# Kernel optimization log

Measured on AMD Instinct MI355X. Metric: run time of the kernel, lower is better.

The kernel has to match this reference:

```python
import jax, jax.numpy as jnp
import numpy as np

N_NODES = 100000
N_EDGES = 1600000
IN_CH = 128
OUT_CH = 128
EDGE_DIM = 6
STATE_DIM = 5


def setup_inputs() -> dict:
    key = jax.random.key(0)
    k = jax.random.split(key, 8)
    x = jax.random.normal(k[0], (N_NODES, IN_CH), dtype=jnp.float32)
    edge_index = jax.random.randint(k[1], (2, N_EDGES), 0, N_NODES, dtype=jnp.int64)
    edge_attr = jax.random.normal(k[2], (N_EDGES, EDGE_DIM), dtype=jnp.float32)
    global_state = jax.random.normal(k[3], (N_NODES, STATE_DIM), dtype=jnp.float32)
    # learned params (glorot init for weights, zero bias like torch default-ish)
    d_neg_in = IN_CH + EDGE_DIM + STATE_DIM
    d_root_in = IN_CH + STATE_DIM
    s_neg = jnp.sqrt(6.0 / (d_neg_in + OUT_CH))
    s_root = jnp.sqrt(6.0 / (d_root_in + OUT_CH))
    W_neg = jax.random.uniform(k[4], (d_neg_in, OUT_CH), jnp.float32, -s_neg, s_neg)
    b_neg = jax.random.uniform(k[5], (OUT_CH,), jnp.float32, -0.05, 0.05)
    W_root = jax.random.uniform(k[6], (d_root_in, OUT_CH), jnp.float32, -s_root, s_root)
    b_root = jax.random.uniform(k[7], (OUT_CH,), jnp.float32, -0.05, 0.05)
    return {"x": x, "edge_index": edge_index, "edge_attr": edge_attr,
            "global_state": global_state, "W_neg": W_neg, "b_neg": b_neg,
            "W_root": W_root, "b_root": b_root}


def reference(x, edge_index, edge_attr, global_state, W_neg, b_neg, W_root, b_root):
    # x: [N, C], global_state: [N, S]
    xs = jnp.concatenate([x, global_state], axis=1)            # [N, C+S]
    src = xs[edge_index[1]]                                    # gather: [E, C+S]
    x_adj = jnp.concatenate([src, edge_attr], axis=1)          # [E, C+S+Ed]
    x_adj = jax.nn.elu(x_adj @ W_neg + b_neg)                  # [E, O]
    neg_sum = jax.ops.segment_sum(x_adj, edge_index[0], num_segments=xs.shape[0])  # [N, O]
    x_out = jax.nn.elu(xs @ W_root + b_root) + neg_sum         # [N, O]
    return x_out
```

## Files before the change

kernel.cpp:

```cpp
#include <hip/hip_runtime.h>
#include <hip/hip_bf16.h>
#include <math.h>

#define N_NODES 100000
#define N_EDGES 1600000
#define IN_CH 128
#define OUT_CH 128
#define EDGE_DIM 6
#define STATE_DIM 5
#define XS_DIM 133
#define KPAD 160
#define NKSTEP 5
#define ASTRIDE 168
#define NBLK 391
#define N_CHUNKS 25000

typedef short s16x8 __attribute__((ext_vector_type(8)));
typedef float f32x4 __attribute__((ext_vector_type(4)));

static __device__ __forceinline__ unsigned short f2bf(float f) {
    __hip_bfloat16 h = __float2bfloat16(f);
    return *reinterpret_cast<unsigned short*>(&h);
}
static __device__ __forceinline__ float bflo(unsigned u) {
    return __uint_as_float(u << 16);
}
static __device__ __forceinline__ float bfhi(unsigned u) {
    return __uint_as_float(u & 0xffff0000u);
}

__global__ __launch_bounds__(64) void repack_w(
    const float* __restrict__ Wneg, const float* __restrict__ Wroot,
    unsigned short* __restrict__ Pneg, unsigned short* __restrict__ Proot)
{
    int b = blockIdx.x;
    int mat = b / 40, r = b % 40;
    int kk = r / 8, nt = r % 8;
    int lane = threadIdx.x;
    const float* W = mat ? Wroot : Wneg;
    unsigned short* P = mat ? Proot : Pneg;
    int n = nt * 16 + (lane & 15);
    int kb = kk * 32 + (lane >> 4) * 8;
    unsigned short v[8];
#pragma unroll
    for (int j = 0; j < 8; ++j) {
        int k = kb + j;
        v[j] = (k < XS_DIM) ? f2bf(W[k * 128 + n]) : (unsigned short)0;
    }
    *(s16x8*)(P + ((size_t)(kk * 8 + nt) * 64 + lane) * 8) = *(s16x8*)v;
}

__global__ __launch_bounds__(256) void node_gemm_mfma(
    const float* __restrict__ x, const float* __restrict__ gs,
    const unsigned short* __restrict__ Pneg, const unsigned short* __restrict__ Proot,
    const float* __restrict__ bneg, const float* __restrict__ broot,
    __hip_bfloat16* __restrict__ Yb, float* __restrict__ out)
{
    __shared__ unsigned short Alds[64 * ASTRIDE];
    const int tid  = threadIdx.x;
    const int lane = tid & 63;
    const int wv   = tid >> 6;
    const int n0   = blockIdx.x * 64;

#pragma unroll
    for (int i = 0; i < 16; ++i) {
        int row = i * 4 + wv;
        int nn  = min(n0 + row, N_NODES - 1);
        const float2 v = *(const float2*)(x + (size_t)nn * IN_CH + lane * 2);
        Alds[row * ASTRIDE + lane * 2]     = f2bf(v.x);
        Alds[row * ASTRIDE + lane * 2 + 1] = f2bf(v.y);
    }
    if (tid < 64) {
        int nn = min(n0 + tid, N_NODES - 1);
#pragma unroll
        for (int j = 0; j < STATE_DIM; ++j)
            Alds[tid * ASTRIDE + IN_CH + j] = f2bf(gs[(size_t)nn * STATE_DIM + j]);
#pragma unroll
        for (int k = XS_DIM; k < KPAD; ++k)
            Alds[tid * ASTRIDE + k] = 0;
    }
    __syncthreads();

    f32x4 accN[8], accR[8];
    const f32x4 zero = {0.f, 0.f, 0.f, 0.f};
#pragma unroll
    for (int nt = 0; nt < 8; ++nt) { accN[nt] = zero; accR[nt] = zero; }

    const int m = lane & 15, quad = lane >> 4;
    const unsigned short* arow = Alds + (wv * 16 + m) * ASTRIDE + quad * 8;

    for (int kk = 0; kk < NKSTEP; ++kk) {
        s16x8 a = *(const s16x8*)(arow + kk * 32);
        const unsigned short* bp = Pneg  + ((size_t)kk * 8 * 64 + lane) * 8;
        const unsigned short* rp = Proot + ((size_t)kk * 8 * 64 + lane) * 8;
#pragma unroll
        for (int nt = 0; nt < 8; ++nt) {
            s16x8 bn = *(const s16x8*)(bp + nt * 512);
            accN[nt] = __builtin_amdgcn_mfma_f32_16x16x32_bf16(a, bn, accN[nt], 0, 0, 0);
            s16x8 br = *(const s16x8*)(rp + nt * 512);
            accR[nt] = __builtin_amdgcn_mfma_f32_16x16x32_bf16(a, br, accR[nt], 0, 0, 0);
        }
    }

#pragma unroll
    for (int nt = 0; nt < 8; ++nt) {
        int col = nt * 16 + m;
        float bn = bneg[col], br = broot[col];
        int rbase = n0 + wv * 16 + quad * 4;
#pragma unroll
        for (int r = 0; r < 4; ++r) {
            int node = rbase + r;
            if (node < N_NODES) {
                Yb[(size_t)node * 128 + col] = __float2bfloat16(accN[nt][r] + bn);
                float v = accR[nt][r] + br;
                out[(size_t)node * 128 + col] = (v > 0.f) ? v : (__expf(v) - 1.f);
            }
        }
    }
}

__global__ __launch_bounds__(256) void histogram(const int* __restrict__ idx,
                                                 int* __restrict__ cnt) {
    int e = blockIdx.x * 256 + threadIdx.x;
    if (e < N_EDGES) atomicAdd(&cnt[idx[e]], 1);
}

__global__ __launch_bounds__(256) void scan_block_sums(const int* __restrict__ cnt,
                                                       int* __restrict__ bsum) {
    __shared__ int ws[4];
    int tid = threadIdx.x, lane = tid & 63, wid = tid >> 6;
    int i = blockIdx.x * 256 + tid;
    int v = (i < N_NODES) ? cnt[i] : 0;
#pragma unroll
    for (int d = 32; d > 0; d >>= 1) v += __shfl_down(v, d);
    if (lane == 0) ws[wid] = v;
    __syncthreads();
    if (tid == 0) bsum[blockIdx.x] = ws[0] + ws[1] + ws[2] + ws[3];
}

__global__ __launch_bounds__(512) void scan_bsums(int* __restrict__ bsum) {
    __shared__ int s[512];
    int tid = threadIdx.x;
    int v = (tid < NBLK) ? bsum[tid] : 0;
    s[tid] = v;
    __syncthreads();
    for (int d = 1; d < 512; d <<= 1) {
        int t = (tid >= d) ? s[tid - d] : 0;
        __syncthreads();
        s[tid] += t;
        __syncthreads();
    }
    if (tid < NBLK) bsum[tid] = s[tid] - v;
}

__global__ __launch_bounds__(256) void scan_final(const int* __restrict__ cnt,
                                                  const int* __restrict__ bsum,
                                                  int* __restrict__ off,
                                                  int* __restrict__ cursor,
                                                  int* __restrict__ chunk_node) {
    __shared__ int wsum[4];
    int tid = threadIdx.x, lane = tid & 63, wid = tid >> 6;
    int i = blockIdx.x * 256 + tid;
    int v = (i < N_NODES) ? cnt[i] : 0;
    int x = v;
#pragma unroll
    for (int d = 1; d < 64; d <<= 1) {
        int t = __shfl_up(x, d);
        if (lane >= d) x += t;
    }
    if (lane == 63) wsum[wid] = x;
    __syncthreads();
    int wpre = 0;
#pragma unroll
    for (int j = 0; j < 4; ++j) wpre += (j < wid) ? wsum[j] : 0;
    int excl = bsum[blockIdx.x] + wpre + x - v;
    if (i < N_NODES) {
        off[i] = excl; cursor[i] = excl;
        if (v > 0) {
            int end = excl + v;
            for (int c = (excl + 63) >> 6; (c << 6) < end; ++c)
                chunk_node[c] = i;
        }
    }
}

__global__ __launch_bounds__(256) void scatter_edges(const int* __restrict__ idx,
                                                     const float* __restrict__ ea,
                                                     int* __restrict__ cursor,
                                                     uint4* __restrict__ pay) {
    int e = blockIdx.x * 256 + threadIdx.x;
    if (e < N_EDGES) {
        int dst = idx[e];
        int src = idx[N_EDGES + e];
        const float* er = ea + (size_t)e * EDGE_DIM;
        unsigned p0 = (unsigned)f2bf(er[0]) | ((unsigned)f2bf(er[1]) << 16);
        unsigned p1 = (unsigned)f2bf(er[2]) | ((unsigned)f2bf(er[3]) << 16);
        unsigned p2 = (unsigned)f2bf(er[4]) | ((unsigned)f2bf(er[5]) << 16);
        int pos = atomicAdd(&cursor[dst], 1);
        uint4 pl = { (unsigned)src, p0, p1, p2 };
        pay[pos] = pl;
    }
}

__global__ __launch_bounds__(256) void aggregate(
    const uint4* __restrict__ pay,
    const float* __restrict__ Wneg,
    const __hip_bfloat16* __restrict__ Yb,
    const int* __restrict__ off,
    const int* __restrict__ chunk_node,
    float* __restrict__ out)
{
    const int lane = threadIdx.x & 63;
    const int wid  = __builtin_amdgcn_readfirstlane(blockIdx.x * 4 + (threadIdx.x >> 6));
    const int e0   = wid * 64;

    const float2* wb2 = (const float2*)(Wneg + 133 * 128);
    float2 wb[EDGE_DIM];
#pragma unroll
    for (int j = 0; j < EDGE_DIM; ++j) wb[j] = wb2[j * 64 + lane];

    const unsigned* Yu = (const unsigned*)Yb;

    uint4 pl = pay[e0 + lane];
    int src_l = (int)pl.x;
    int ea0 = (int)pl.y, ea1 = (int)pl.z, ea2 = (int)pl.w;

    int n   = __builtin_amdgcn_readfirstlane(chunk_node[wid]);
    int nxt = __builtin_amdgcn_readfirstlane((n + 1 < N_NODES) ? off[n + 1] : N_EDGES);

    float accx = 0.f, accy = 0.f;

    unsigned yA[8], yB[8];
#pragma unroll
    for (int j = 0; j < 8; ++j) {
        int s = __builtin_amdgcn_readlane(src_l, j);
        yA[j] = Yu[(size_t)s * 64 + lane];
    }
#pragma unroll
    for (int j = 0; j < 8; ++j) {
        int s = __builtin_amdgcn_readlane(src_l, 8 + j);
        yB[j] = Yu[(size_t)s * 64 + lane];
    }

    auto edge_op = [&](unsigned yv, int c, bool last) {
        unsigned a0 = (unsigned)__builtin_amdgcn_readlane(ea0, c);
        unsigned a1 = (unsigned)__builtin_amdgcn_readlane(ea1, c);
        unsigned a2 = (unsigned)__builtin_amdgcn_readlane(ea2, c);
        float f0 = bflo(a0), f1 = bfhi(a0);
        float f2 = bflo(a1), f3 = bfhi(a1);
        float f4 = bflo(a2), f5 = bfhi(a2);
        float tx = bflo(yv), ty = bfhi(yv);
        tx = fmaf(f0, wb[0].x, tx); ty = fmaf(f0, wb[0].y, ty);
        tx = fmaf(f1, wb[1].x, tx); ty = fmaf(f1, wb[1].y, ty);
        tx = fmaf(f2, wb[2].x, tx); ty = fmaf(f2, wb[2].y, ty);
        tx = fmaf(f3, wb[3].x, tx); ty = fmaf(f3, wb[3].y, ty);
        tx = fmaf(f4, wb[4].x, tx); ty = fmaf(f4, wb[4].y, ty);
        tx = fmaf(f5, wb[5].x, tx); ty = fmaf(f5, wb[5].y, ty);
        tx = (tx > 0.f) ? tx : (__expf(tx) - 1.f);
        ty = (ty > 0.f) ? ty : (__expf(ty) - 1.f);
        accx += tx; accy += ty;
        int e = e0 + c;
        bool bend = (e + 1 == nxt);
        if (last || bend) {
            float* orow = out + (size_t)n * 128 + (lane << 1);
            atomicAdd(orow,     accx);
            atomicAdd(orow + 1, accy);
            accx = 0.f; accy = 0.f;
            if (!last) {
                n++;
                nxt = __builtin_amdgcn_readfirstlane(
                    (n + 1 < N_NODES) ? off[n + 1] : N_EDGES);
                while (nxt <= e + 1) {
                    n++;
                    nxt = __builtin_amdgcn_readfirstlane(
                        (n + 1 < N_NODES) ? off[n + 1] : N_EDGES);
                }
            }
        }
    };

#pragma unroll 1
    for (int q = 0; q < 3; ++q) {
        const int base = q * 16;
        const int pb   = base + 16;
#pragma unroll
        for (int j = 0; j < 8; ++j) {
            edge_op(yA[j], base + j, false);
            int s = __builtin_amdgcn_readlane(src_l, pb + j);
            yA[j] = Yu[(size_t)s * 64 + lane];
        }
#pragma unroll
        for (int j = 0; j < 8; ++j) {
            edge_op(yB[j], base + 8 + j, false);
            int s = __builtin_amdgcn_readlane(src_l, pb + 8 + j);
            yB[j] = Yu[(size_t)s * 64 + lane];
        }
    }
#pragma unroll
    for (int j = 0; j < 8; ++j) edge_op(yA[j], 48 + j, false);
#pragma unroll
    for (int j = 0; j < 8; ++j) edge_op(yB[j], 56 + j, j == 7);
}

extern "C" void kernel_launch(void* const* d_in, const int* in_sizes, int n_in,
                              void* d_out, int out_size, void* d_ws, size_t ws_size,
                              hipStream_t stream) {
    const float* x     = (const float*)d_in[0];
    const int*   idx   = (const int*)  d_in[1];
    const float* ea    = (const float*)d_in[2];
    const float* gs    = (const float*)d_in[3];
    const float* Wneg  = (const float*)d_in[4];
    const float* bneg  = (const float*)d_in[5];
    const float* Wroot = (const float*)d_in[6];
    const float* broot = (const float*)d_in[7];
    float* out = (float*)d_out;

    char* w = (char*)d_ws;
    __hip_bfloat16* Yb = (__hip_bfloat16*)w;      w += (size_t)N_NODES * 128 * 2;
    int* cnt  = (int*)w;                          w += (size_t)N_NODES * 4;
    int* off  = (int*)w;                          w += (size_t)N_NODES * 4;
    int* cur  = (int*)w;                          w += (size_t)N_NODES * 4;
    int* bsum = (int*)w;                          w += 2048;
    uint4* pay = (uint4*)w;                       w += (size_t)N_EDGES * 16;
    unsigned short* Pneg  = (unsigned short*)w;   w += (size_t)NKSTEP * 8 * 64 * 8 * 2;
    unsigned short* Proot = (unsigned short*)w;   w += (size_t)NKSTEP * 8 * 64 * 8 * 2;
    int* chunk_node = (int*)w;

    const int nb_edges = (N_EDGES + 255) / 256;

    repack_w<<<80, 64, 0, stream>>>(Wneg, Wroot, Pneg, Proot);
    node_gemm_mfma<<<(N_NODES + 63) / 64, 256, 0, stream>>>(
        x, gs, Pneg, Proot, bneg, broot, Yb, out);
    hipMemsetAsync(cnt, 0, (size_t)N_NODES * 4, stream);
    histogram<<<nb_edges, 256, 0, stream>>>(idx, cnt);
    scan_block_sums<<<NBLK, 256, 0, stream>>>(cnt, bsum);
    scan_bsums<<<1, 512, 0, stream>>>(bsum);
    scan_final<<<NBLK, 256, 0, stream>>>(cnt, bsum, off, cur, chunk_node);
    scatter_edges<<<nb_edges, 256, 0, stream>>>(idx, ea, cur, pay);
    aggregate<<<N_CHUNKS / 4, 256, 0, stream>>>(pay, Wneg, Yb, off, chunk_node, out);
}
```

Before: 451.4 us.

## Fuse degree histogram into node GEMM kernel via interleaved block roles

Merges the node GEMM and the destination histogram into a single launch where even and odd blocks take GEMM and histogram roles, so the atomic counting overlaps with the MFMA work and one launch is removed. It also adds nontemporal loads and stores for streaming data (x, indices, edge attributes, payload) and packs the LDS staging writes into 32-bit stores, with global_state and zero padding spread across all threads. The risks are that interleaving roles changes occupancy and cache behaviour, and that the nontemporal hints may hurt if the payload would otherwise stay resident in L2 for the aggregate kernel.

```diff
diff --git a/kernel.cpp b/kernel.cpp
--- a/kernel.cpp
+++ b/kernel.cpp
@@ -14,9 +14,13 @@
 #define ASTRIDE 168
 #define NBLK 391
 #define N_CHUNKS 25000
+#define NGB 1563
+#define NHB 1601
 
 typedef short s16x8 __attribute__((ext_vector_type(8)));
 typedef float f32x4 __attribute__((ext_vector_type(4)));
+typedef float f32x2 __attribute__((ext_vector_type(2)));
+typedef unsigned u32x4 __attribute__((ext_vector_type(4)));
 
 static __device__ __forceinline__ unsigned short f2bf(float f) {
     __hip_bfloat16 h = __float2bfloat16(f);
@@ -50,34 +54,52 @@
     *(s16x8*)(P + ((size_t)(kk * 8 + nt) * 64 + lane) * 8) = *(s16x8*)v;
 }
 
-__global__ __launch_bounds__(256) void node_gemm_mfma(
+__global__ __launch_bounds__(256) void gemm_hist(
     const float* __restrict__ x, const float* __restrict__ gs,
     const unsigned short* __restrict__ Pneg, const unsigned short* __restrict__ Proot,
     const float* __restrict__ bneg, const float* __restrict__ broot,
-    __hip_bfloat16* __restrict__ Yb, float* __restrict__ out)
+    __hip_bfloat16* __restrict__ Yb, float* __restrict__ out,
+    const int* __restrict__ idx, int* __restrict__ cnt)
 {
     __shared__ unsigned short Alds[64 * ASTRIDE];
+    const int bid = blockIdx.x;
+    int role, rid;
+    if (bid < 2 * NGB) { role = bid & 1; rid = bid >> 1; }
+    else               { role = 1;       rid = NGB + (bid - 2 * NGB); }
+
     const int tid  = threadIdx.x;
+
+    if (role == 1) {
+        for (int e = rid * 256 + tid; e < N_EDGES; e += NHB * 256) {
+            int d = __builtin_nontemporal_load(idx + e);
+            atomicAdd(&cnt[d], 1);
+        }
+        return;
+    }
+
     const int lane = tid & 63;
     const int wv   = tid >> 6;
-    const int n0   = blockIdx.x * 64;
+    const int n0   = rid * 64;
 
 #pragma unroll
     for (int i = 0; i < 16; ++i) {
         int row = i * 4 + wv;
         int nn  = min(n0 + row, N_NODES - 1);
-        const float2 v = *(const float2*)(x + (size_t)nn * IN_CH + lane * 2);
-        Alds[row * ASTRIDE + lane * 2]     = f2bf(v.x);
-        Alds[row * ASTRIDE + lane * 2 + 1] = f2bf(v.y);
-    }
-    if (tid < 64) {
-        int nn = min(n0 + tid, N_NODES - 1);
-#pragma unroll
-        for (int j = 0; j < STATE_DIM; ++j)
-            Alds[tid * ASTRIDE + IN_CH + j] = f2bf(gs[(size_t)nn * STATE_DIM + j]);
-#pragma unroll
-        for (int k = XS_DIM; k < KPAD; ++k)
-            Alds[tid * ASTRIDE + k] = 0;
+        const f32x2 v = __builtin_nontemporal_load(
+            (const f32x2*)(x + (size_t)nn * IN_CH) + lane);
+        unsigned pk = (unsigned)f2bf(v.x) | ((unsigned)f2bf(v.y) << 16);
+        *(unsigned*)(&Alds[row * ASTRIDE + lane * 2]) = pk;
+    }
+#pragma unroll
+    for (int s2 = 0; s2 < 4; ++s2) {
+        int slot = tid * 4 + s2;
+        int row  = slot >> 4;
+        int cp   = slot & 15;
+        int nn   = min(n0 + row, N_NODES - 1);
+        int c0   = IN_CH + cp * 2;
+        unsigned lo = (c0     < XS_DIM) ? (unsigned)f2bf(gs[(size_t)nn * STATE_DIM + (c0 - IN_CH)])     : 0u;
+        unsigned hi = (c0 + 1 < XS_DIM) ? (unsigned)f2bf(gs[(size_t)nn * STATE_DIM + (c0 + 1 - IN_CH)]) : 0u;
+        *(unsigned*)(&Alds[row * ASTRIDE + c0]) = lo | (hi << 16);
     }
     __syncthreads();
 
@@ -117,12 +139,6 @@
             }
         }
     }
-}
-
-__global__ __launch_bounds__(256) void histogram(const int* __restrict__ idx,
-                                                 int* __restrict__ cnt) {
-    int e = blockIdx.x * 256 + threadIdx.x;
-    if (e < N_EDGES) atomicAdd(&cnt[idx[e]], 1);
 }
 
 __global__ __launch_bounds__(256) void scan_block_sums(const int* __restrict__ cnt,
@@ -190,15 +206,18 @@
                                                      uint4* __restrict__ pay) {
     int e = blockIdx.x * 256 + threadIdx.x;
     if (e < N_EDGES) {
-        int dst = idx[e];
-        int src = idx[N_EDGES + e];
-        const float* er = ea + (size_t)e * EDGE_DIM;
-        unsigned p0 = (unsigned)f2bf(er[0]) | ((unsigned)f2bf(er[1]) << 16);
-        unsigned p1 = (unsigned)f2bf(er[2]) | ((unsigned)f2bf(er[3]) << 16);
-        unsigned p2 = (unsigned)f2bf(er[4]) | ((unsigned)f2bf(er[5]) << 16);
+        int dst = __builtin_nontemporal_load(idx + e);
+        int src = __builtin_nontemporal_load(idx + N_EDGES + e);
+        const f32x2* er = (const f32x2*)(ea + (size_t)e * EDGE_DIM);
+        f32x2 e01 = __builtin_nontemporal_load(er);
+        f32x2 e23 = __builtin_nontemporal_load(er + 1);
+        f32x2 e45 = __builtin_nontemporal_load(er + 2);
+        unsigned p0 = (unsigned)f2bf(e01.x) | ((unsigned)f2bf(e01.y) << 16);
+        unsigned p1 = (unsigned)f2bf(e23.x) | ((unsigned)f2bf(e23.y) << 16);
+        unsigned p2 = (unsigned)f2bf(e45.x) | ((unsigned)f2bf(e45.y) << 16);
         int pos = atomicAdd(&cursor[dst], 1);
-        uint4 pl = { (unsigned)src, p0, p1, p2 };
-        pay[pos] = pl;
+        u32x4 pl = { (unsigned)src, p0, p1, p2 };
+        __builtin_nontemporal_store(pl, (u32x4*)pay + pos);
     }
 }
 
@@ -221,7 +240,7 @@
 
     const unsigned* Yu = (const unsigned*)Yb;
 
-    uint4 pl = pay[e0 + lane];
+    u32x4 pl = __builtin_nontemporal_load((const u32x4*)pay + e0 + lane);
     int src_l = (int)pl.x;
     int ea0 = (int)pl.y, ea1 = (int)pl.z, ea2 = (int)pl.w;
 
@@ -262,7 +281,7 @@
         int e = e0 + c;
         bool bend = (e + 1 == nxt);
         if (last || bend) {
-            float* orow = out + (size_t)n * 128 + (lane << 1);
+            float* orow = out + ((size_t)n << 7) + (lane << 1);
             atomicAdd(orow,     accx);
             atomicAdd(orow + 1, accy);
             accx = 0.f; accy = 0.f;
@@ -328,11 +347,10 @@
 
     const int nb_edges = (N_EDGES + 255) / 256;
 
+    hipMemsetAsync(cnt, 0, (size_t)N_NODES * 4, stream);
     repack_w<<<80, 64, 0, stream>>>(Wneg, Wroot, Pneg, Proot);
-    node_gemm_mfma<<<(N_NODES + 63) / 64, 256, 0, stream>>>(
-        x, gs, Pneg, Proot, bneg, broot, Yb, out);
-    hipMemsetAsync(cnt, 0, (size_t)N_NODES * 4, stream);
-    histogram<<<nb_edges, 256, 0, stream>>>(idx, cnt);
+    gemm_hist<<<2 * NGB + (NHB - NGB), 256, 0, stream>>>(
+        x, gs, Pneg, Proot, bneg, broot, Yb, out, idx, cnt);
     scan_block_sums<<<NBLK, 256, 0, stream>>>(cnt, bsum);
     scan_bsums<<<1, 512, 0, stream>>>(bsum);
     scan_final<<<NBLK, 256, 0, stream>>>(cnt, bsum, off, cur, chunk_node);
```

Result: faster. 433.7 us (-3.9%).
